# Kernel optimization log

Hardware: AMD Instinct MI355X
Metric: run time of the kernel (lower is better)

Reference implementation:

```python
import jax, jax.numpy as jnp
import numpy as np

N_NODES = 50000
HID = 64
EPS = 1e-5
POS_COLS = np.array([0, 1, 14])  # pos_x, pos_y, battery


def setup_inputs() -> dict:
    key = jax.random.key(0)
    ks = jax.random.split(key, 10)
    x = jax.random.normal(ks[0], (N_NODES, 16), dtype=jnp.float32)
    edge_index = jax.random.randint(ks[1], (2, 1600000), 0, N_NODES, dtype=jnp.int64)
    # 6 structurally identical conv layers: Linear(6,64) -> ReLU -> Linear(64,64)
    W1 = jax.random.normal(ks[2], (6, 6, HID), dtype=jnp.float32) * (1.0 / np.sqrt(6))
    b1 = jax.random.normal(ks[3], (6, HID), dtype=jnp.float32) * 0.02
    W2 = jax.random.normal(ks[4], (6, HID, HID), dtype=jnp.float32) * (1.0 / np.sqrt(HID))
    b2 = jax.random.normal(ks[5], (6, HID), dtype=jnp.float32) * 0.02
    # 5 BatchNorm layers (training mode: batch statistics over nodes)
    bn_gamma = jnp.ones((5, HID), dtype=jnp.float32) + 0.1 * jax.random.normal(ks[6], (5, HID), dtype=jnp.float32)
    bn_beta = 0.1 * jax.random.normal(ks[7], (5, HID), dtype=jnp.float32)
    return {"x": x, "edge_index": edge_index, "W1": W1, "b1": b1,
            "W2": W2, "b2": b2, "bn_gamma": bn_gamma, "bn_beta": bn_beta}


def _conv(x, src, dst, W1, b1, W2, b2):
    # pos_battery = x[:, [0,1,14]]; message = MLP(cat(x_j - x_i, x_i)); aggr='add' at target i
    p = x[:, POS_COLS]                       # [N, 3]
    x_i = p[dst]                             # targets  [E, 3]
    x_j = p[src]                             # sources  [E, 3]
    m = jnp.concatenate([x_j - x_i, x_i], axis=1)   # [E, 6]
    h = jax.nn.relu(m @ W1 + b1) @ W2 + b2          # [E, HID]
    return jax.ops.segment_sum(h, dst, num_segments=x.shape[0])


def _bn(h, gamma, beta):
    mu = jnp.mean(h, axis=0)
    var = jnp.var(h, axis=0)  # biased, matching BatchNorm training normalization
    return (h - mu) * jax.lax.rsqrt(var + EPS) * gamma + beta


def reference(x, edge_index, W1, b1, W2, b2, bn_gamma, bn_beta):
    n = x.shape[0]
    loop = jnp.arange(n, dtype=edge_index.dtype)
    src = jnp.concatenate([edge_index[0], loop])   # add_self_loops (done per layer in torch,
    dst = jnp.concatenate([edge_index[1], loop])   # identical result every layer)
    h = x
    for l in range(6):
        h = _conv(h, src, dst, W1[l], b1[l], W2[l], b2[l])
        if l < 5:
            h = jax.nn.relu(_bn(h, bn_gamma[l], bn_beta[l]))
    return h
```

## Files before the change

### kernel.cpp

```cpp
#include <hip/hip_runtime.h>
#include <hip/hip_fp16.h>
#include <cstdint>

#define NN 50000
#define NQBLK8 1563
#define NGBLK2 6250
#define EPSV 1e-5f

#define NPB 128
#define BSH 7
#define NBKT 391
#define CHUNK 4096
#define EPT 16
#define LDSE 6144

#define NSLOT 128

typedef unsigned short ushort_t;
typedef _Float16 half2v __attribute__((ext_vector_type(2)));

__global__ __launch_bounds__(256) void k_hist1(const int* __restrict__ dst, int E, int nchunk,
                                               int* __restrict__ hist, float* __restrict__ gsumsp) {
    __shared__ int cnt[NBKT];
    int t = threadIdx.x, blk = blockIdx.x;
    if (blk == 0) {
        for (int z = t; z < 5 * NSLOT * 8; z += 256) gsumsp[z] = 0.f;
    }
    for (int b = t; b < NBKT; b += 256) cnt[b] = 0;
    __syncthreads();
    int base = blk * CHUNK;
#pragma unroll
    for (int k = 0; k < EPT; ++k) {
        int e = base + k * 256 + t;
        if (e < E) atomicAdd(&cnt[dst[e] >> BSH], 1);
    }
    __syncthreads();
    for (int b = t; b < NBKT; b += 256) hist[(size_t)b * nchunk + blk] = cnt[b];
}

__global__ __launch_bounds__(256) void k_scanA(const int* __restrict__ in, int n,
                                               int* __restrict__ presum, int* __restrict__ blocksum) {
    __shared__ int lds[256];
    int t = threadIdx.x, g = blockIdx.x * 256 + t;
    int v = (g < n) ? in[g] : 0;
    lds[t] = v;
    __syncthreads();
    for (int off = 1; off < 256; off <<= 1) {
        int x = (t >= off) ? lds[t - off] : 0;
        __syncthreads();
        lds[t] += x;
        __syncthreads();
    }
    if (g < n) presum[g] = lds[t];
    if (t == 255) blocksum[blockIdx.x] = lds[255];
}

__global__ __launch_bounds__(256) void k_scanC(const int* __restrict__ presum,
                                               const int* __restrict__ hist,
                                               const int* __restrict__ blocksum,
                                               int n, int nchunk, int* __restrict__ offsT) {
    __shared__ int lds[256];
    int t = threadIdx.x, myblk = blockIdx.x;
    int acc = 0;
    for (int i = t; i < myblk; i += 256) acc += blocksum[i];
    lds[t] = acc;
    __syncthreads();
    for (int off = 128; off > 0; off >>= 1) {
        if (t < off) lds[t] += lds[t + off];
        __syncthreads();
    }
    int boff = lds[0];
    int g = myblk * 256 + t;
    if (g < n) {
        int val = presum[g] - hist[g] + boff;
        int b = g / nchunk;
        int c = g - b * nchunk;
        offsT[(size_t)c * NBKT + b] = val;
    }
}

__global__ __launch_bounds__(256) void k_scatter1(const int* __restrict__ src,
                                                  const int* __restrict__ dst, int E,
                                                  const int* __restrict__ offsT,
                                                  int* __restrict__ ebuf) {
    __shared__ int pos[NBKT];
    int t = threadIdx.x, blk = blockIdx.x;
    for (int b = t; b < NBKT; b += 256) pos[b] = offsT[(size_t)blk * NBKT + b];
    __syncthreads();
    int base = blk * CHUNK;
#pragma unroll
    for (int k = 0; k < EPT; ++k) {
        int e = base + k * 256 + t;
        if (e < E) {
            int d = dst[e];
            int b = d >> BSH;
            int p = atomicAdd(&pos[b], 1);
            ebuf[p] = ((d & (NPB - 1)) << 16) | src[e];
        }
    }
}

__global__ __launch_bounds__(256) void k_bucket_csr(const int* __restrict__ ebuf,
                                                    const int* __restrict__ offsT, int E,
                                                    int* __restrict__ rowstart,
                                                    ushort_t* __restrict__ colsrc) {
    __shared__ int cnt[NPB];
    __shared__ int s[NPB];
    __shared__ int pos2[NPB];
    __shared__ ushort_t lout[LDSE];
    int t = threadIdx.x, b = blockIdx.x;
    int bstart = offsT[b];
    int bend = (b + 1 < NBKT) ? offsT[b + 1] : E;
    int m = bend - bstart;
    if (t < NPB) cnt[t] = 0;
    __syncthreads();
    for (int i = bstart + t; i < bend; i += 256) atomicAdd(&cnt[ebuf[i] >> 16], 1);
    __syncthreads();
    if (t < NPB) s[t] = cnt[t];
    __syncthreads();
    for (int off = 1; off < NPB; off <<= 1) {
        int x = (t < NPB && t >= off) ? s[t - off] : 0;
        __syncthreads();
        if (t < NPB) s[t] += x;
        __syncthreads();
    }
    if (t < NPB) {
        int excl = s[t] - cnt[t];
        int node = b * NPB + t;
        if (node < NN) rowstart[node] = bstart + excl;
        pos2[t] = excl;
    }
    __syncthreads();
    if (m <= LDSE) {
        for (int i = bstart + t; i < bend; i += 256) {
            int v = ebuf[i];
            int p = atomicAdd(&pos2[v >> 16], 1);
            lout[p] = (ushort_t)(v & 0xFFFF);
        }
        __syncthreads();
        for (int i = t; i < m; i += 256) colsrc[bstart + i] = lout[i];
    } else {
        for (int i = bstart + t; i < bend; i += 256) {
            int v = ebuf[i];
            int p = atomicAdd(&pos2[v >> 16], 1);
            colsrc[bstart + p] = (ushort_t)(v & 0xFFFF);
        }
    }
    if (b == NBKT - 1 && t == 0) rowstart[NN] = E;
}

__global__ __launch_bounds__(256) void k_q(
    const float* __restrict__ pin, int pstride, int c0, int c1, int c2,
    const float* __restrict__ W1l, const float* __restrict__ b1l,
    const float* __restrict__ gsum_prev, const float* __restrict__ gamma_l,
    const float* __restrict__ beta_l, int use_bn,
    __half* __restrict__ qs, __half* __restrict__ qd) {
    __shared__ float red[6][8];
    __shared__ float scv[3], shv[3];
    int tid = threadIdx.x;
    if (use_bn) {
        if (tid < 48) {
            int j = tid >> 3, k = tid & 7;
            float s = 0.f;
            for (int slot = k; slot < NSLOT; slot += 8) s += gsum_prev[slot * 8 + j];
            red[j][k] = s;
        }
        __syncthreads();
        if (tid < 3) {
            const int cols[3] = {0, 1, 14};
            float sum = 0.f, sumsq = 0.f;
#pragma unroll
            for (int k2 = 0; k2 < 8; ++k2) { sum += red[tid][k2]; sumsq += red[tid + 3][k2]; }
            float mu = sum / (float)NN;
            float var = sumsq / (float)NN - mu * mu;
            float rs = rsqrtf(var + EPSV);
            float g = gamma_l[cols[tid]];
            scv[tid] = rs * g;
            shv[tid] = beta_l[cols[tid]] - mu * rs * g;
        }
        __syncthreads();
    }
    int idx = blockIdx.x * 256 + tid;
    int v = idx >> 3, g = idx & 7;
    if (v >= NN) return;
    const float* prow = pin + (size_t)v * pstride;
    float p0 = prow[c0], p1 = prow[c1], p2 = prow[c2];
    if (use_bn) {
        p0 = fmaxf(0.f, p0 * scv[0] + shv[0]);
        p1 = fmaxf(0.f, p1 * scv[1] + shv[1]);
        p2 = fmaxf(0.f, p2 * scv[2] + shv[2]);
    }
    unsigned int us[4], ud[4];
#pragma unroll
    for (int pr = 0; pr < 4; ++pr) {
        int c = (g << 3) + (pr << 1);
        float w0a = W1l[c], w1a = W1l[64 + c], w2a = W1l[128 + c];
        float qsa = p0 * w0a + p1 * w1a + p2 * w2a;
        float qda = p0 * (W1l[192 + c] - w0a) + p1 * (W1l[256 + c] - w1a)
                  + p2 * (W1l[320 + c] - w2a) + b1l[c];
        int c1i = c + 1;
        float w0b = W1l[c1i], w1b = W1l[64 + c1i], w2b = W1l[128 + c1i];
        float qsb = p0 * w0b + p1 * w1b + p2 * w2b;
        float qdb = p0 * (W1l[192 + c1i] - w0b) + p1 * (W1l[256 + c1i] - w1b)
                  + p2 * (W1l[320 + c1i] - w2b) + b1l[c1i];
        us[pr] = (unsigned int)__half_as_ushort(__float2half(qsa))
               | ((unsigned int)__half_as_ushort(__float2half(qsb)) << 16);
        ud[pr] = (unsigned int)__half_as_ushort(__float2half(qda))
               | ((unsigned int)__half_as_ushort(__float2half(qdb)) << 16);
    }
    uint4 vs = {us[0], us[1], us[2], us[3]};
    uint4 vd = {ud[0], ud[1], ud[2], ud[3]};
    ((uint4*)qs)[(size_t)v * 8 + g] = vs;
    ((uint4*)qd)[(size_t)v * 8 + g] = vd;
}

__device__ __forceinline__ half2v bitcast_h2(unsigned int u) {
    union { unsigned int u; half2v h; } cvt;
    cvt.u = u;
    return cvt.h;
}

__device__ __forceinline__ void accum8f(const char* __restrict__ qsb, unsigned int byteoff,
                                        const half2v qd2[4], float acc[8]) {
    uint4 q = *reinterpret_cast<const uint4*>(qsb + byteoff);
    unsigned int wd[4] = {q.x, q.y, q.z, q.w};
    const half2v z2 = {(_Float16)0.0f, (_Float16)0.0f};
#pragma unroll
    for (int d = 0; d < 4; ++d) {
        half2v r = bitcast_h2(wd[d]) + qd2[d];
        r = __builtin_elementwise_max(r, z2);
        acc[2 * d]     += (float)r.x;
        acc[2 * d + 1] += (float)r.y;
    }
}

__device__ __forceinline__ void chunk_math32(const uint4 q[4], const half2v qd2[4],
                                             int r, int es, float acc[8]) {
    const half2v z2 = {(_Float16)0.0f, (_Float16)0.0f};
    half2v h[4] = {z2, z2, z2, z2};
#pragma unroll
    for (int k = 0; k < 4; ++k) {
        bool ok = ((k << 3) + es) < r;
        unsigned int wd[4] = {q[k].x, q[k].y, q[k].z, q[k].w};
#pragma unroll
        for (int d = 0; d < 4; ++d) {
            half2v t = bitcast_h2(wd[d]) + qd2[d];
            t = __builtin_elementwise_max(t, z2);
            h[d] += ok ? t : z2;
        }
    }
#pragma unroll
    for (int d = 0; d < 4; ++d) {
        acc[2 * d]     += (float)h[d].x;
        acc[2 * d + 1] += (float)h[d].y;
    }
}

__device__ __forceinline__ int clamp32(int x) { return x < 32 ? (x < 0 ? 0 : x) : 32; }

__device__ __forceinline__ void pair_edge_loop(const char* __restrict__ qsb,
                                               const ushort_t* __restrict__ colsrc,
                                               int iA, int e0, int iB, int e1,
                                               int lane, int es, unsigned int cg16,
                                               const half2v qd2A[4], const half2v qd2B[4],
                                               float accA[8], float accB[8]) {
    int rA = clamp32(e0 - iA);
    int rB = clamp32(e1 - iB);
    if (rA == 0 && rB == 0) return;
    int slA = (lane < rA) ? (int)colsrc[iA + lane] : 0;
    int slB = (lane < rB) ? (int)colsrc[iB + lane] : 0;
    while (true) {
        uint4 qA[4], qB[4];
#pragma unroll
        for (int k = 0; k < 4; ++k) {
            int s = __shfl(slA, (k << 3) + es);
            qA[k] = *reinterpret_cast<const uint4*>(qsb + (((unsigned int)(s << 7)) | cg16));
        }
#pragma unroll
        for (int k = 0; k < 4; ++k) {
            int s = __shfl(slB, (k << 3) + es);
            qB[k] = *reinterpret_cast<const uint4*>(qsb + (((unsigned int)(s << 7)) | cg16));
        }
        int iA2 = iA + rA, iB2 = iB + rB;
        int rA2 = clamp32(e0 - iA2);
        int rB2 = clamp32(e1 - iB2);
        bool more = (rA2 > 0) || (rB2 > 0);
        int slA2 = 0, slB2 = 0;
        if (more) {
            slA2 = (lane < rA2) ? (int)colsrc[iA2 + lane] : 0;
            slB2 = (lane < rB2) ? (int)colsrc[iB2 + lane] : 0;
        }
        chunk_math32(qA, qd2A, rA, es, accA);
        chunk_math32(qB, qd2B, rB, es, accB);
        if (!more) break;
        iA = iA2; iB = iB2; rA = rA2; rB = rB2; slA = slA2; slB = slB2;
    }
}

__global__ __launch_bounds__(256, 4) void k_gather3(
    const __half* __restrict__ qs, const __half* __restrict__ qd,
    const int* __restrict__ rowstart, const ushort_t* __restrict__ colsrc,
    const float* __restrict__ W2l, const float* __restrict__ b2l,
    float* __restrict__ pnext, float* __restrict__ gsum_l) {
    __shared__ float w2c[3][64];
    __shared__ float b2c[3];
    __shared__ float part[4][8];
    int tid = threadIdx.x;
    if (tid < 192) {
        int cj = tid >> 6;
        int col = (cj == 0) ? 0 : ((cj == 1) ? 1 : 14);
        w2c[cj][tid & 63] = W2l[(tid & 63) * 64 + col];
    }
    if (tid < 3) b2c[tid] = b2l[(tid == 0) ? 0 : ((tid == 1) ? 1 : 14)];
    __syncthreads();

    int w = tid >> 6, lane = tid & 63;
    int es = lane >> 3, cg = lane & 7;
    unsigned int cg16 = (unsigned int)(cg << 4);
    int v0 = (blockIdx.x * 4 + w) * 2;
    const char* qsb = (const char*)qs;

    uint4 qqA = ((const uint4*)qd)[(size_t)v0 * 8 + cg];
    uint4 qqB = ((const uint4*)qd)[(size_t)(v0 + 1) * 8 + cg];
    half2v qd2A[4], qd2B[4];
    {
        unsigned int qa[4] = {qqA.x, qqA.y, qqA.z, qqA.w};
        unsigned int qb[4] = {qqB.x, qqB.y, qqB.z, qqB.w};
#pragma unroll
        for (int d = 0; d < 4; ++d) { qd2A[d] = bitcast_h2(qa[d]); qd2B[d] = bitcast_h2(qb[d]); }
    }

    float accA[8] = {0, 0, 0, 0, 0, 0, 0, 0};
    float accB[8] = {0, 0, 0, 0, 0, 0, 0, 0};
    int s0 = rowstart[v0], e0 = rowstart[v0 + 1], e1 = rowstart[v0 + 2];
    if (es == 0) {
        accum8f(qsb, ((unsigned int)(v0 << 7)) | cg16, qd2A, accA);
        accum8f(qsb, ((unsigned int)((v0 + 1) << 7)) | cg16, qd2B, accB);
    }
    pair_edge_loop(qsb, colsrc, s0, e0, e0, e1, lane, es, cg16, qd2A, qd2B, accA, accB);

    float degA = (float)(e0 - s0 + 1);
    float degB = (float)(e1 - e0 + 1);
#pragma unroll
    for (int j = 0; j < 3; ++j) {
        float tA = 0.f, tB = 0.f;
#pragma unroll
        for (int k = 0; k < 8; ++k) {
            float wv = w2c[j][cg * 8 + k];
            tA += accA[k] * wv;
            tB += accB[k] * wv;
        }
        tA += __shfl_xor(tA, 1);  tB += __shfl_xor(tB, 1);
        tA += __shfl_xor(tA, 2);  tB += __shfl_xor(tB, 2);
        tA += __shfl_xor(tA, 4);  tB += __shfl_xor(tB, 4);
        tA += __shfl_xor(tA, 8);  tB += __shfl_xor(tB, 8);
        tA += __shfl_xor(tA, 16); tB += __shfl_xor(tB, 16);
        tA += __shfl_xor(tA, 32); tB += __shfl_xor(tB, 32);
        if (lane == 0) {
            float valA = tA + degA * b2c[j];
            float valB = tB + degB * b2c[j];
            pnext[v0 * 3 + j] = valA;
            pnext[(v0 + 1) * 3 + j] = valB;
            part[w][j] = valA + valB;
            part[w][3 + j] = valA * valA + valB * valB;
        }
    }
    __syncthreads();
    if (tid < 6) {
        float ssum = part[0][tid] + part[1][tid] + part[2][tid] + part[3][tid];
        atomicAdd(&gsum_l[(blockIdx.x & (NSLOT - 1)) * 8 + tid], ssum);
    }
}

__global__ __launch_bounds__(256, 4) void k_gather_full(
    const __half* __restrict__ qs, const __half* __restrict__ qd,
    const int* __restrict__ rowstart, const ushort_t* __restrict__ colsrc,
    const float* __restrict__ W2l, const float* __restrict__ b2l,
    float* __restrict__ out) {
    __shared__ float lds[4][2][64];
    int tid = threadIdx.x;
    int w = tid >> 6, lane = tid & 63;
    int es = lane >> 3, cg = lane & 7;
    unsigned int cg16 = (unsigned int)(cg << 4);
    int v0 = (blockIdx.x * 4 + w) * 2;
    const char* qsb = (const char*)qs;

    uint4 qqA = ((const uint4*)qd)[(size_t)v0 * 8 + cg];
    uint4 qqB = ((const uint4*)qd)[(size_t)(v0 + 1) * 8 + cg];
    half2v qd2A[4], qd2B[4];
    {
        unsigned int qa[4] = {qqA.x, qqA.y, qqA.z, qqA.w};
        unsigned int qb[4] = {qqB.x, qqB.y, qqB.z, qqB.w};
#pragma unroll
        for (int d = 0; d < 4; ++d) { qd2A[d] = bitcast_h2(qa[d]); qd2B[d] = bitcast_h2(qb[d]); }
    }

    float accA[8] = {0, 0, 0, 0, 0, 0, 0, 0};
    float accB[8] = {0, 0, 0, 0, 0, 0, 0, 0};
    int s0 = rowstart[v0], e0 = rowstart[v0 + 1], e1 = rowstart[v0 + 2];
    if (es == 0) {
        accum8f(qsb, ((unsigned int)(v0 << 7)) | cg16, qd2A, accA);
        accum8f(qsb, ((unsigned int)((v0 + 1) << 7)) | cg16, qd2B, accB);
    }
    pair_edge_loop(qsb, colsrc, s0, e0, e0, e1, lane, es, cg16, qd2A, qd2B, accA, accB);

#pragma unroll
    for (int k = 0; k < 8; ++k) {
        accA[k] += __shfl_xor(accA[k], 8);
        accA[k] += __shfl_xor(accA[k], 16);
        accA[k] += __shfl_xor(accA[k], 32);
        accB[k] += __shfl_xor(accB[k], 8);
        accB[k] += __shfl_xor(accB[k], 16);
        accB[k] += __shfl_xor(accB[k], 32);
    }
    if (es == 0) {
#pragma unroll
        for (int k = 0; k < 8; ++k) {
            lds[w][0][cg * 8 + k] = accA[k];
            lds[w][1][cg * 8 + k] = accB[k];
        }
    }
    __syncthreads();
    float degA = (float)(e0 - s0 + 1);
    float degB = (float)(e1 - e0 + 1);
    float bl = b2l[lane];
    float sumA = degA * bl;
    float sumB = degB * bl;
    for (int k = 0; k < 64; ++k) {
        float wv = W2l[k * 64 + lane];
        sumA += lds[w][0][k] * wv;
        sumB += lds[w][1][k] * wv;
    }
    out[(size_t)v0 * 64 + lane] = sumA;
    out[(size_t)(v0 + 1) * 64 + lane] = sumB;
}


static inline size_t align_up(size_t x) { return (x + 255) & ~(size_t)255; }

extern "C" void kernel_launch(void* const* d_in, const int* in_sizes, int n_in,
                              void* d_out, int out_size, void* d_ws, size_t ws_size,
                              hipStream_t stream) {
    const float* x     = (const float*)d_in[0];
    const int*   ei    = (const int*)d_in[1];
    const float* W1    = (const float*)d_in[2];
    const float* b1    = (const float*)d_in[3];
    const float* W2    = (const float*)d_in[4];
    const float* b2    = (const float*)d_in[5];
    const float* gamma = (const float*)d_in[6];
    const float* beta  = (const float*)d_in[7];
    float* out = (float*)d_out;
    const int E = in_sizes[1] / 2;
    const int* src = ei;
    const int* dst = ei + E;

    const int nchunk = (E + CHUNK - 1) / CHUNK;
    const int nscan  = NBKT * nchunk;
    const int nsb    = (nscan + 255) / 256;

    char* base = (char*)d_ws;
    size_t off = 0;
    __half* qs = (__half*)(base + off);     off = align_up(off + (size_t)NN * 64 * 2);
    __half* qd = (__half*)(base + off);     off = align_up(off + (size_t)NN * 64 * 2);
    float* pA = (float*)(base + off);       off = align_up(off + (size_t)NN * 3 * 4);
    float* pB = (float*)(base + off);       off = align_up(off + (size_t)NN * 3 * 4);
    int* rowstart = (int*)(base + off);     off = align_up(off + (size_t)(NN + 1) * 4);
    ushort_t* colsrc = (ushort_t*)(base + off); off = align_up(off + (size_t)E * 2);
    int* ebuf     = (int*)(base + off);     off = align_up(off + (size_t)E * 4);
    int* hist     = (int*)(base + off);     off = align_up(off + (size_t)nscan * 4);
    int* offsT    = (int*)(base + off);     off = align_up(off + (size_t)nscan * 4);
    int* presum   = (int*)(base + off);     off = align_up(off + (size_t)nscan * 4);
    int* bsum     = (int*)(base + off);     off = align_up(off + (size_t)nsb * 4);
    float* gsumsp = (float*)(base + off);   off = align_up(off + (size_t)5 * NSLOT * 8 * 4);
    (void)ws_size; (void)n_in; (void)out_size;

    k_hist1<<<nchunk, 256, 0, stream>>>(dst, E, nchunk, hist, gsumsp);
    k_scanA<<<nsb, 256, 0, stream>>>(hist, nscan, presum, bsum);
    k_scanC<<<nsb, 256, 0, stream>>>(presum, hist, bsum, nscan, nchunk, offsT);
    k_scatter1<<<nchunk, 256, 0, stream>>>(src, dst, E, offsT, ebuf);
    k_bucket_csr<<<NBKT, 256, 0, stream>>>(ebuf, offsT, E, rowstart, colsrc);

    float* pc = pA;
    float* pn = pB;
    for (int l = 0; l < 6; ++l) {
        const float* pin = (l == 0) ? x : pc;
        int pstride = (l == 0) ? 16 : 3;
        int c0 = 0, c1 = 1, c2 = (l == 0) ? 14 : 2;
        const float* gsum_prev = (l == 0) ? gsumsp : gsumsp + (size_t)(l - 1) * NSLOT * 8;
        const float* gamma_prev = (l == 0) ? gamma : gamma + (size_t)(l - 1) * 64;
        const float* beta_prev  = (l == 0) ? beta  : beta  + (size_t)(l - 1) * 64;
        k_q<<<NQBLK8, 256, 0, stream>>>(pin, pstride, c0, c1, c2,
                                        W1 + (size_t)l * 6 * 64, b1 + (size_t)l * 64,
                                        gsum_prev, gamma_prev, beta_prev,
                                        (l > 0) ? 1 : 0, qs, qd);
        if (l < 5) {
            k_gather3<<<NGBLK2, 256, 0, stream>>>(qs, qd, rowstart, colsrc,
                                                  W2 + (size_t)l * 64 * 64, b2 + (size_t)l * 64,
                                                  pn, gsumsp + (size_t)l * NSLOT * 8);
            float* tmp = pc; pc = pn; pn = tmp;
        } else {
            k_gather_full<<<NGBLK2, 256, 0, stream>>>(qs, qd, rowstart, colsrc,
                                                      W2 + (size_t)5 * 64 * 64, b2 + (size_t)5 * 64,
                                                      out);
        }
    }
}
```

Before: 404.6 us.

## Process four nodes per wavefront with 16-edge chunks in gather kernels

Each wavefront in the gather kernels now handles four destination nodes instead of two. Each node gets 16 lanes of edge indices per chunk instead of 32, and the grid is halved. With about 33 edges per node, this should waste fewer lanes on partially filled 32-edge chunks and put more independent loads in flight per iteration. The cost is higher register pressure (four accumulator sets), and the launch_bounds occupancy hint has been dropped, which may lower occupancy.

Measured after the change: 395.1 us. 1.02x faster.

```diff
diff --git a/kernel.cpp b/kernel.cpp
--- a/kernel.cpp
+++ b/kernel.cpp
@@ -4,7 +4,7 @@
 
 #define NN 50000
 #define NQBLK8 1563
-#define NGBLK2 6250
+#define NGBLK4 3125
 #define EPSV 1e-5f
 
 #define NPB 128
@@ -234,12 +234,12 @@
     }
 }
 
-__device__ __forceinline__ void chunk_math32(const uint4 q[4], const half2v qd2[4],
+__device__ __forceinline__ void chunk_math16(const uint4 q[2], const half2v qd2[4],
                                              int r, int es, float acc[8]) {
     const half2v z2 = {(_Float16)0.0f, (_Float16)0.0f};
     half2v h[4] = {z2, z2, z2, z2};
 #pragma unroll
-    for (int k = 0; k < 4; ++k) {
+    for (int k = 0; k < 2; ++k) {
         bool ok = ((k << 3) + es) < r;
         unsigned int wd[4] = {q[k].x, q[k].y, q[k].z, q[k].w};
 #pragma unroll
@@ -256,48 +256,68 @@
     }
 }
 
-__device__ __forceinline__ int clamp32(int x) { return x < 32 ? (x < 0 ? 0 : x) : 32; }
-
-__device__ __forceinline__ void pair_edge_loop(const char* __restrict__ qsb,
+__device__ __forceinline__ int clamp16(int x) { return x < 16 ? (x < 0 ? 0 : x) : 16; }
+
+__device__ __forceinline__ void quad_edge_loop(const char* __restrict__ qsb,
                                                const ushort_t* __restrict__ colsrc,
-                                               int iA, int e0, int iB, int e1,
+                                               int i0, int e0, int i1, int e1,
+                                               int i2, int e2, int i3, int e3,
                                                int lane, int es, unsigned int cg16,
-                                               const half2v qd2A[4], const half2v qd2B[4],
-                                               float accA[8], float accB[8]) {
-    int rA = clamp32(e0 - iA);
-    int rB = clamp32(e1 - iB);
-    if (rA == 0 && rB == 0) return;
-    int slA = (lane < rA) ? (int)colsrc[iA + lane] : 0;
-    int slB = (lane < rB) ? (int)colsrc[iB + lane] : 0;
+                                               const half2v qd2a[4], const half2v qd2b[4],
+                                               const half2v qd2c[4], const half2v qd2d[4],
+                                               float accA[8], float accB[8],
+                                               float accC[8], float accD[8]) {
+    int r0 = clamp16(e0 - i0), r1 = clamp16(e1 - i1);
+    int r2 = clamp16(e2 - i2), r3 = clamp16(e3 - i3);
+    if ((r0 | r1 | r2 | r3) == 0) return;
+    int g = lane >> 4, o = lane & 15;
+    int isel = (g == 0) ? i0 : (g == 1) ? i1 : (g == 2) ? i2 : i3;
+    int rsel = (g == 0) ? r0 : (g == 1) ? r1 : (g == 2) ? r2 : r3;
+    int sl = (o < rsel) ? (int)colsrc[isel + o] : 0;
     while (true) {
-        uint4 qA[4], qB[4];
-#pragma unroll
-        for (int k = 0; k < 4; ++k) {
-            int s = __shfl(slA, (k << 3) + es);
+        uint4 qA[2], qB[2], qC[2], qD[2];
+#pragma unroll
+        for (int k = 0; k < 2; ++k) {
+            int s = __shfl(sl, 0 * 16 + (k << 3) + es);
             qA[k] = *reinterpret_cast<const uint4*>(qsb + (((unsigned int)(s << 7)) | cg16));
         }
 #pragma unroll
-        for (int k = 0; k < 4; ++k) {
-            int s = __shfl(slB, (k << 3) + es);
+        for (int k = 0; k < 2; ++k) {
+            int s = __shfl(sl, 1 * 16 + (k << 3) + es);
             qB[k] = *reinterpret_cast<const uint4*>(qsb + (((unsigned int)(s << 7)) | cg16));
         }
-        int iA2 = iA + rA, iB2 = iB + rB;
-        int rA2 = clamp32(e0 - iA2);
-        int rB2 = clamp32(e1 - iB2);
-        bool more = (rA2 > 0) || (rB2 > 0);
-        int slA2 = 0, slB2 = 0;
+#pragma unroll
+        for (int k = 0; k < 2; ++k) {
+            int s = __shfl(sl, 2 * 16 + (k << 3) + es);
+            qC[k] = *reinterpret_cast<const uint4*>(qsb + (((unsigned int)(s << 7)) | cg16));
+        }
+#pragma unroll
+        for (int k = 0; k < 2; ++k) {
+            int s = __shfl(sl, 3 * 16 + (k << 3) + es);
+            qD[k] = *reinterpret_cast<const uint4*>(qsb + (((unsigned int)(s << 7)) | cg16));
+        }
+        int j0 = i0 + r0, j1 = i1 + r1, j2 = i2 + r2, j3 = i3 + r3;
+        int n0 = clamp16(e0 - j0), n1 = clamp16(e1 - j1);
+        int n2 = clamp16(e2 - j2), n3 = clamp16(e3 - j3);
+        bool more = (n0 | n1 | n2 | n3) != 0;
+        int sl2 = 0;
         if (more) {
-            slA2 = (lane < rA2) ? (int)colsrc[iA2 + lane] : 0;
-            slB2 = (lane < rB2) ? (int)colsrc[iB2 + lane] : 0;
-        }
-        chunk_math32(qA, qd2A, rA, es, accA);
-        chunk_math32(qB, qd2B, rB, es, accB);
+            int isel2 = (g == 0) ? j0 : (g == 1) ? j1 : (g == 2) ? j2 : j3;
+            int rsel2 = (g == 0) ? n0 : (g == 1) ? n1 : (g == 2) ? n2 : n3;
+            sl2 = (o < rsel2) ? (int)colsrc[isel2 + o] : 0;
+        }
+        chunk_math16(qA, qd2a, r0, es, accA);
+        chunk_math16(qB, qd2b, r1, es, accB);
+        chunk_math16(qC, qd2c, r2, es, accC);
+        chunk_math16(qD, qd2d, r3, es, accD);
         if (!more) break;
-        iA = iA2; iB = iB2; rA = rA2; rB = rB2; slA = slA2; slB = slB2;
-    }
-}
-
-__global__ __launch_bounds__(256, 4) void k_gather3(
+        i0 = j0; i1 = j1; i2 = j2; i3 = j3;
+        r0 = n0; r1 = n1; r2 = n2; r3 = n3;
+        sl = sl2;
+    }
+}
+
+__global__ __launch_bounds__(256) void k_gather3(
     const __half* __restrict__ qs, const __half* __restrict__ qd,
     const int* __restrict__ rowstart, const ushort_t* __restrict__ colsrc,
     const float* __restrict__ W2l, const float* __restrict__ b2l,
@@ -317,52 +337,70 @@
     int w = tid >> 6, lane = tid & 63;
     int es = lane >> 3, cg = lane & 7;
     unsigned int cg16 = (unsigned int)(cg << 4);
-    int v0 = (blockIdx.x * 4 + w) * 2;
+    int v0 = (blockIdx.x * 4 + w) * 4;
     const char* qsb = (const char*)qs;
 
-    uint4 qqA = ((const uint4*)qd)[(size_t)v0 * 8 + cg];
-    uint4 qqB = ((const uint4*)qd)[(size_t)(v0 + 1) * 8 + cg];
-    half2v qd2A[4], qd2B[4];
+    half2v qd2a[4], qd2b[4], qd2c[4], qd2d[4];
     {
-        unsigned int qa[4] = {qqA.x, qqA.y, qqA.z, qqA.w};
-        unsigned int qb[4] = {qqB.x, qqB.y, qqB.z, qqB.w};
-#pragma unroll
-        for (int d = 0; d < 4; ++d) { qd2A[d] = bitcast_h2(qa[d]); qd2B[d] = bitcast_h2(qb[d]); }
-    }
-
-    float accA[8] = {0, 0, 0, 0, 0, 0, 0, 0};
-    float accB[8] = {0, 0, 0, 0, 0, 0, 0, 0};
-    int s0 = rowstart[v0], e0 = rowstart[v0 + 1], e1 = rowstart[v0 + 2];
+        uint4 qA = ((const uint4*)qd)[(size_t)v0 * 8 + cg];
+        uint4 qB = ((const uint4*)qd)[(size_t)(v0 + 1) * 8 + cg];
+        uint4 qC = ((const uint4*)qd)[(size_t)(v0 + 2) * 8 + cg];
+        uint4 qD = ((const uint4*)qd)[(size_t)(v0 + 3) * 8 + cg];
+        unsigned int ua[4] = {qA.x, qA.y, qA.z, qA.w};
+        unsigned int ub[4] = {qB.x, qB.y, qB.z, qB.w};
+        unsigned int uc[4] = {qC.x, qC.y, qC.z, qC.w};
+        unsigned int ud[4] = {qD.x, qD.y, qD.z, qD.w};
+#pragma unroll
+        for (int d = 0; d < 4; ++d) {
+            qd2a[d] = bitcast_h2(ua[d]); qd2b[d] = bitcast_h2(ub[d]);
+            qd2c[d] = bitcast_h2(uc[d]); qd2d[d] = bitcast_h2(ud[d]);
+        }
+    }
+
+    float accA[8] = {0,0,0,0,0,0,0,0};
+    float accB[8] = {0,0,0,0,0,0,0,0};
+    float accC[8] = {0,0,0,0,0,0,0,0};
+    float accD[8] = {0,0,0,0,0,0,0,0};
+    int rs0 = rowstart[v0], rs1 = rowstart[v0 + 1], rs2 = rowstart[v0 + 2];
+    int rs3 = rowstart[v0 + 3], rs4 = rowstart[v0 + 4];
     if (es == 0) {
-        accum8f(qsb, ((unsigned int)(v0 << 7)) | cg16, qd2A, accA);
-        accum8f(qsb, ((unsigned int)((v0 + 1) << 7)) | cg16, qd2B, accB);
-    }
-    pair_edge_loop(qsb, colsrc, s0, e0, e0, e1, lane, es, cg16, qd2A, qd2B, accA, accB);
-
-    float degA = (float)(e0 - s0 + 1);
-    float degB = (float)(e1 - e0 + 1);
+        accum8f(qsb, ((unsigned int)(v0 << 7)) | cg16, qd2a, accA);
+        accum8f(qsb, ((unsigned int)((v0 + 1) << 7)) | cg16, qd2b, accB);
+        accum8f(qsb, ((unsigned int)((v0 + 2) << 7)) | cg16, qd2c, accC);
+        accum8f(qsb, ((unsigned int)((v0 + 3) << 7)) | cg16, qd2d, accD);
+    }
+    quad_edge_loop(qsb, colsrc, rs0, rs1, rs1, rs2, rs2, rs3, rs3, rs4,
+                   lane, es, cg16, qd2a, qd2b, qd2c, qd2d, accA, accB, accC, accD);
+
+    float degA = (float)(rs1 - rs0 + 1);
+    float degB = (float)(rs2 - rs1 + 1);
+    float degC = (float)(rs3 - rs2 + 1);
+    float degD = (float)(rs4 - rs3 + 1);
 #pragma unroll
     for (int j = 0; j < 3; ++j) {
-        float tA = 0.f, tB = 0.f;
+        float tA = 0.f, tB = 0.f, tC = 0.f, tD = 0.f;
 #pragma unroll
         for (int k = 0; k < 8; ++k) {
             float wv = w2c[j][cg * 8 + k];
-            tA += accA[k] * wv;
-            tB += accB[k] * wv;
-        }
-        tA += __shfl_xor(tA, 1);  tB += __shfl_xor(tB, 1);
-        tA += __shfl_xor(tA, 2);  tB += __shfl_xor(tB, 2);
-        tA += __shfl_xor(tA, 4);  tB += __shfl_xor(tB, 4);
-        tA += __shfl_xor(tA, 8);  tB += __shfl_xor(tB, 8);
-        tA += __shfl_xor(tA, 16); tB += __shfl_xor(tB, 16);
-        tA += __shfl_xor(tA, 32); tB += __shfl_xor(tB, 32);
+            tA += accA[k] * wv; tB += accB[k] * wv;
+            tC += accC[k] * wv; tD += accD[k] * wv;
+        }
+#pragma unroll
+        for (int st = 1; st <= 32; st <<= 1) {
+            tA += __shfl_xor(tA, st); tB += __shfl_xor(tB, st);
+            tC += __shfl_xor(tC, st); tD += __shfl_xor(tD, st);
+        }
         if (lane == 0) {
-            float valA = tA + degA * b2c[j];
-            float valB = tB + degB * b2c[j];
-            pnext[v0 * 3 + j] = valA;
-            pnext[(v0 + 1) * 3 + j] = valB;
-            part[w][j] = valA + valB;
-            part[w][3 + j] = valA * valA + valB * valB;
+            float vA = tA + degA * b2c[j];
+            float vB = tB + degB * b2c[j];
+            float vC = tC + degC * b2c[j];
+            float vD = tD + degD * b2c[j];
+            pnext[v0 * 3 + j] = vA;
+            pnext[(v0 + 1) * 3 + j] = vB;
+            pnext[(v0 + 2) * 3 + j] = vC;
+            pnext[(v0 + 3) * 3 + j] = vD;
+            part[w][j] = vA + vB + vC + vD;
+            part[w][3 + j] = vA * vA + vB * vB + vC * vC + vD * vD;
         }
     }
     __syncthreads();
@@ -372,67 +410,87 @@
     }
 }
 
-__global__ __launch_bounds__(256, 4) void k_gather_full(
+__global__ __launch_bounds__(256) void k_gather_full(
     const __half* __restrict__ qs, const __half* __restrict__ qd,
     const int* __restrict__ rowstart, const ushort_t* __restrict__ colsrc,
     const float* __restrict__ W2l, const float* __restrict__ b2l,
     float* __restrict__ out) {
-    __shared__ float lds[4][2][64];
+    __shared__ float lds[4][4][64];
     int tid = threadIdx.x;
     int w = tid >> 6, lane = tid & 63;
     int es = lane >> 3, cg = lane & 7;
     unsigned int cg16 = (unsigned int)(cg << 4);
-    int v0 = (blockIdx.x * 4 + w) * 2;
+    int v0 = (blockIdx.x * 4 + w) * 4;
     const char* qsb = (const char*)qs;
 
-    uint4 qqA = ((const uint4*)qd)[(size_t)v0 * 8 + cg];
-    uint4 qqB = ((const uint4*)qd)[(size_t)(v0 + 1) * 8 + cg];
-    half2v qd2A[4], qd2B[4];
+    half2v qd2a[4], qd2b[4], qd2c[4], qd2d[4];
     {
-        unsigned int qa[4] = {qqA.x, qqA.y, qqA.z, qqA.w};
-        unsigned int qb[4] = {qqB.x, qqB.y, qqB.z, qqB.w};
-#pragma unroll
-        for (int d = 0; d < 4; ++d) { qd2A[d] = bitcast_h2(qa[d]); qd2B[d] = bitcast_h2(qb[d]); }
-    }
-
-    float accA[8] = {0, 0, 0, 0, 0, 0, 0, 0};
-    float accB[8] = {0, 0, 0, 0, 0, 0, 0, 0};
-    int s0 = rowstart[v0], e0 = rowstart[v0 + 1], e1 = rowstart[v0 + 2];
+        uint4 qA = ((const uint4*)qd)[(size_t)v0 * 8 + cg];
+        uint4 qB = ((const uint4*)qd)[(size_t)(v0 + 1) * 8 + cg];
+        uint4 qC = ((const uint4*)qd)[(size_t)(v0 + 2) * 8 + cg];
+        uint4 qD = ((const uint4*)qd)[(size_t)(v0 + 3) * 8 + cg];
+        unsigned int ua[4] = {qA.x, qA.y, qA.z, qA.w};
+        unsigned int ub[4] = {qB.x, qB.y, qB.z, qB.w};
+        unsigned int uc[4] = {qC.x, qC.y, qC.z, qC.w};
+        unsigned int ud[4] = {qD.x, qD.y, qD.z, qD.w};
+#pragma unroll
+        for (int d = 0; d < 4; ++d) {
+            qd2a[d] = bitcast_h2(ua[d]); qd2b[d] = bitcast_h2(ub[d]);
+            qd2c[d] = bitcast_h2(uc[d]); qd2d[d] = bitcast_h2(ud[d]);
+        }
+    }
+
+    float accA[8] = {0,0,0,0,0,0,0,0};
+    float accB[8] = {0,0,0,0,0,0,0,0};
+    float accC[8] = {0,0,0,0,0,0,0,0};
+    float accD[8] = {0,0,0,0,0,0,0,0};
+    int rs0 = rowstart[v0], rs1 = rowstart[v0 + 1], rs2 = rowstart[v0 + 2];
+    int rs3 = rowstart[v0 + 3], rs4 = rowstart[v0 + 4];
     if (es == 0) {
-        accum8f(qsb, ((unsigned int)(v0 << 7)) | cg16, qd2A, accA);
-        accum8f(qsb, ((unsigned int)((v0 + 1) << 7)) | cg16, qd2B, accB);
-    }
-    pair_edge_loop(qsb, colsrc, s0, e0, e0, e1, lane, es, cg16, qd2A, qd2B, accA, accB);
+        accum8f(qsb, ((unsigned int)(v0 << 7)) | cg16, qd2a, accA);
+        accum8f(qsb, ((unsigned int)((v0 + 1) << 7)) | cg16, qd2b, accB);
+        accum8f(qsb, ((unsigned int)((v0 + 2) << 7)) | cg16, qd2c, accC);
+        accum8f(qsb, ((unsigned int)((v0 + 3) << 7)) | cg16, qd2d, accD);
+    }
+    quad_edge_loop(qsb, colsrc, rs0, rs1, rs1, rs2, rs2, rs3, rs3, rs4,
+                   lane, es, cg16, qd2a, qd2b, qd2c, qd2d, accA, accB, accC, accD);
 
 #pragma unroll
     for (int k = 0; k < 8; ++k) {
-        accA[k] += __shfl_xor(accA[k], 8);
-        accA[k] += __shfl_xor(accA[k], 16);
-        accA[k] += __shfl_xor(accA[k], 32);
-        accB[k] += __shfl_xor(accB[k], 8);
-        accB[k] += __shfl_xor(accB[k], 16);
-        accB[k] += __shfl_xor(accB[k], 32);
+#pragma unroll
+        for (int st = 8; st <= 32; st <<= 1) {
+            accA[k] += __shfl_xor(accA[k], st);
+            accB[k] += __shfl_xor(accB[k], st);
+            accC[k] += __shfl_xor(accC[k], st);
+            accD[k] += __shfl_xor(accD[k], st);
+        }
     }
     if (es == 0) {
 #pragma unroll
         for (int k = 0; k < 8; ++k) {
             lds[w][0][cg * 8 + k] = accA[k];
             lds[w][1][cg * 8 + k] = accB[k];
-        }
-    }
-    __syncthreads();
-    float degA = (float)(e0 - s0 + 1);
-    float degB = (float)(e1 - e0 + 1);
+            lds[w][2][cg * 8 + k] = accC[k];
+            lds[w][3][cg * 8 + k] = accD[k];
+        }
+    }
+    __syncthreads();
     float bl = b2l[lane];
-    float sumA = degA * bl;
-    float sumB = degB * bl;
+    float sumA = (float)(rs1 - rs0 + 1) * bl;
+    float sumB = (float)(rs2 - rs1 + 1) * bl;
+    float sumC = (float)(rs3 - rs2 + 1) * bl;
+    float sumD = (float)(rs4 - rs3 + 1) * bl;
     for (int k = 0; k < 64; ++k) {
         float wv = W2l[k * 64 + lane];
         sumA += lds[w][0][k] * wv;
         sumB += lds[w][1][k] * wv;
+        sumC += lds[w][2][k] * wv;
+        sumD += lds[w][3][k] * wv;
     }
     out[(size_t)v0 * 64 + lane] = sumA;
     out[(size_t)(v0 + 1) * 64 + lane] = sumB;
+    out[(size_t)(v0 + 2) * 64 + lane] = sumC;
+    out[(size_t)(v0 + 3) * 64 + lane] = sumD;
 }
 
 
@@ -494,12 +552,12 @@
                                         gsum_prev, gamma_prev, beta_prev,
                                         (l > 0) ? 1 : 0, qs, qd);
         if (l < 5) {
-            k_gather3<<<NGBLK2, 256, 0, stream>>>(qs, qd, rowstart, colsrc,
+            k_gather3<<<NGBLK4, 256, 0, stream>>>(qs, qd, rowstart, colsrc,
                                                   W2 + (size_t)l * 64 * 64, b2 + (size_t)l * 64,
                                                   pn, gsumsp + (size_t)l * NSLOT * 8);
             float* tmp = pc; pc = pn; pn = tmp;
         } else {
-            k_gather_full<<<NGBLK2, 256, 0, stream>>>(qs, qd, rowstart, colsrc,
+            k_gather_full<<<NGBLK4, 256, 0, stream>>>(qs, qd, rowstart, colsrc,
                                                       W2 + (size_t)5 * 64 * 64, b2 + (size_t)5 * 64,
                                                       out);
         }
```
